# Kernel optimization log

Hardware: AMD Instinct MI355X
Metric: run time of the kernel (lower is better)

The kernel has to match this reference:

```python
import jax, jax.numpy as jnp
import numpy as np

N_NODES = 100000
N_EDGES = 1600000
NUM_FEATURES = 64
HIDDEN = 64
NUM_CLASSES = 16


def setup_inputs() -> dict:
    key = jax.random.key(0)
    ks = jax.random.split(key, 8)
    x = jax.random.normal(ks[0], (N_NODES, NUM_FEATURES), dtype=jnp.float32)
    edge_index = jax.random.randint(ks[1], (2, N_EDGES), 0, N_NODES, dtype=jnp.int32)
    # Glorot-ish init for weights, zero bias (matches GCNConv / Linear defaults closely enough)
    s1 = 1.0 / np.sqrt(NUM_FEATURES)
    s2 = 1.0 / np.sqrt(HIDDEN)
    W1 = jax.random.uniform(ks[2], (NUM_FEATURES, HIDDEN), jnp.float32, -s1, s1)
    b1 = jnp.zeros((HIDDEN,), jnp.float32)
    W2 = jax.random.uniform(ks[3], (HIDDEN, HIDDEN), jnp.float32, -s2, s2)
    b2 = jnp.zeros((HIDDEN,), jnp.float32)
    W3 = jax.random.uniform(ks[4], (HIDDEN, NUM_CLASSES), jnp.float32, -s2, s2)
    b3 = jax.random.uniform(ks[5], (NUM_CLASSES,), jnp.float32, -s2, s2)
    return {"x": x, "edge_index": edge_index, "W1": W1, "b1": b1,
            "W2": W2, "b2": b2, "W3": W3, "b3": b3}


def _gcn_layer(x, W, b, src, dst, norm, n_nodes):
    # GCNConv: h = X W; out[i] = sum_{(j->i)} norm_ji * h[j]; out += b
    h = x @ W                                   # [N, H] small dense GEMM
    msg = h[src] * norm[:, None]                # [E+N, H] irregular gather
    out = jax.ops.segment_sum(msg, dst, num_segments=n_nodes)  # scatter-add
    return out + b


def reference(x, edge_index, W1, b1, W2, b2, W3, b3):
    n = x.shape[0]
    loop = jnp.arange(n, dtype=edge_index.dtype)
    # add self-loops (PyG GCNConv default add_self_loops=True)
    src = jnp.concatenate([edge_index[0], loop])
    dst = jnp.concatenate([edge_index[1], loop])
    # symmetric normalization D^{-1/2} A_hat D^{-1/2}
    deg = jax.ops.segment_sum(jnp.ones_like(src, dtype=x.dtype), dst, num_segments=n)
    dis = jax.lax.rsqrt(deg)                    # deg >= 1 due to self-loops
    norm = dis[src] * dis[dst]                  # [E+N]

    h = jax.nn.relu(_gcn_layer(x, W1, b1, src, dst, norm, n))
    # F.dropout(training=False) -> identity (module in eval mode)
    h = jax.nn.relu(_gcn_layer(h, W2, b2, src, dst, norm, n))
    z = h @ W3 + b3
    return jax.nn.log_softmax(z, axis=1), h
```

## Files before the change

### kernel.cpp

```cpp
#include <hip/hip_runtime.h>
#include <hip/hip_bf16.h>

typedef __hip_bfloat16 bf16;
typedef unsigned short ushort;

#define NN 100000
#define NE 1600000
#define NBKT 391
#define BCAP 4608
#define EPB 4096
#define NP1 391
#define NMT 6250

typedef __attribute__((ext_vector_type(8))) short s8v;
typedef __attribute__((ext_vector_type(4))) float f4v;

__device__ __forceinline__ float ldf(const void* p, int i, int f32) {
    return f32 ? ((const float*)p)[i] : __bfloat162float(((const bf16*)p)[i]);
}
__device__ __forceinline__ void stf(void* p, int i, int f32, float v) {
    if (f32) ((float*)p)[i] = v;
    else     ((bf16*)p)[i] = __float2bfloat16(v);
}

__device__ __forceinline__ ushort f2b(float f) {
    unsigned u = __builtin_bit_cast(unsigned, f);
    u += 0x7FFF + ((u >> 16) & 1);
    return (ushort)(u >> 16);
}
__device__ __forceinline__ float b2f(ushort h) {
    unsigned u = ((unsigned)h) << 16;
    return __builtin_bit_cast(float, u);
}
__device__ __forceinline__ float blo(unsigned u) {
    return __builtin_bit_cast(float, u << 16);
}
__device__ __forceinline__ float bhi(unsigned u) {
    return __builtin_bit_cast(float, u & 0xffff0000u);
}

__global__ void k_detect(const unsigned* __restrict__ x, int* __restrict__ flag) {
    __shared__ int cnt[256];
    int t = threadIdx.x, c = 0;
    for (int i = t; i < 2048; i += 256) {
        unsigned e7 = (x[i] >> 8) & 0x7F;
        c += (e7 >= 60 && e7 <= 66) ? 1 : 0;
    }
    cnt[t] = c;
    __syncthreads();
    for (int s = 128; s > 0; s >>= 1) {
        if (t < s) cnt[t] += cnt[t + s];
        __syncthreads();
    }
    if (t == 0) *flag = (cnt[0] >= 1024) ? 0 : 1;
}

__global__ void k_sentinel(unsigned* out) {
    if (threadIdx.x == 0 && blockIdx.x == 0) out[0] = 0x461C461Cu;
}

__global__ void k_cnt(const int* __restrict__ dst, int* __restrict__ cnt) {
    __shared__ int hist[NBKT];
    int b = blockIdx.x, t = threadIdx.x;
    for (int i = t; i < NBKT; i += 256) hist[i] = 0;
    __syncthreads();
    int e0 = b * EPB;
#pragma unroll
    for (int k = 0; k < EPB; k += 256) {
        int e = e0 + k + t;
        if (e < NE) atomicAdd(&hist[dst[e] >> 8], 1);
    }
    __syncthreads();
    for (int i = t; i < NBKT; i += 256) cnt[b * NBKT + i] = hist[i];
}

__global__ void k_colscan(const int* __restrict__ cnt, int* __restrict__ prefT,
                          int* __restrict__ btot) {
    __shared__ int s[512];
    int k = blockIdx.x, t = threadIdx.x;
    int v = (t < NP1) ? cnt[t * NBKT + k] : 0;
    s[t] = v;
    __syncthreads();
    for (int d = 1; d < 512; d <<= 1) {
        int add = (t >= d) ? s[t - d] : 0;
        __syncthreads();
        s[t] += add;
        __syncthreads();
    }
    if (t < NP1) prefT[k * NP1 + t] = s[t] - v;
    if (t == 511) btot[k] = s[511];
}

__global__ void k_scanB(const int* __restrict__ btot, int* __restrict__ gbase,
                        int* __restrict__ rowptr) {
    __shared__ int s[512];
    int t = threadIdx.x;
    int v = (t < NBKT) ? btot[t] : 0;
    s[t] = v;
    __syncthreads();
    for (int d = 1; d < 512; d <<= 1) {
        int add = (t >= d) ? s[t - d] : 0;
        __syncthreads();
        s[t] += add;
        __syncthreads();
    }
    if (t < NBKT) gbase[t] = s[t] - v;
    if (t == 0) { gbase[NBKT] = NE; rowptr[NN] = NE; }
}

__global__ void k_place(const int* __restrict__ src, const int* __restrict__ dst,
                        const int* __restrict__ prefT, unsigned* __restrict__ bbuf) {
    __shared__ int base[NBKT];
    __shared__ int lcur[NBKT];
    int b = blockIdx.x, t = threadIdx.x;
    for (int i = t; i < NBKT; i += 256) {
        base[i] = prefT[i * NP1 + b];
        lcur[i] = 0;
    }
    __syncthreads();
    int e0 = b * EPB;
#pragma unroll
    for (int k = 0; k < EPB; k += 256) {
        int e = e0 + k + t;
        if (e < NE) {
            int d = dst[e];
            int kb = d >> 8;
            int lp = atomicAdd(&lcur[kb], 1);
            bbuf[kb * BCAP + base[kb] + lp] = ((unsigned)src[e] << 8) | (unsigned)(d & 255);
        }
    }
}

__global__ void k_pass2(const unsigned* __restrict__ bbuf, const int* __restrict__ gbase,
                        int* __restrict__ rowptr, float* __restrict__ dis,
                        int* __restrict__ csr_off) {
    __shared__ unsigned vals[BCAP];
    __shared__ int lout[BCAP];
    __shared__ int fh[256], fx[256], fc[256];
    int b = blockIdx.x, t = threadIdx.x;
    int g0 = gbase[b], cntb = gbase[b + 1] - g0;
    const unsigned* in = bbuf + b * BCAP;
    fh[t] = 0;
    __syncthreads();
    for (int i = t; i < cntb; i += 256) {
        unsigned v = in[i];
        vals[i] = v;
        atomicAdd(&fh[v & 255], 1);
    }
    __syncthreads();
    fx[t] = fh[t];
    __syncthreads();
    for (int d = 1; d < 256; d <<= 1) {
        int add = (t >= d) ? fx[t - d] : 0;
        __syncthreads();
        fx[t] += add;
        __syncthreads();
    }
    int n = b * 256 + t;
    int ex = fx[t] - fh[t];
    fc[t] = ex;
    if (n < NN) {
        rowptr[n] = g0 + ex;
        dis[n] = rsqrtf(1.0f + (float)fh[t]);
    }
    __syncthreads();
    for (int i = t; i < cntb; i += 256) {
        unsigned v = vals[i];
        int p = atomicAdd(&fc[v & 255], 1);
        lout[p] = (int)((v >> 8) << 7);
    }
    __syncthreads();
    for (int i = t; i < cntb; i += 256) csr_off[g0 + i] = lout[i];
}

__global__ void __launch_bounds__(256) k_gemm_mfma(
        const void* __restrict__ A, int aBase, const void* __restrict__ W,
        bf16* __restrict__ C, const float* __restrict__ dis,
        const int* __restrict__ flag) {
    int f32 = *flag;
    int t = threadIdx.x;
    if (blockIdx.x == 0 && t < 64) ((ushort*)C)[NN * 64 + t] = 0;
    int lane = t & 63;
    int w = t >> 6;
    int m = lane & 15, q = lane >> 4;

    s8v bh[2][4], bl[2][4];
#pragma unroll
    for (int st = 0; st < 2; st++)
#pragma unroll
        for (int nt = 0; nt < 4; nt++)
#pragma unroll
            for (int j = 0; j < 8; j++) {
                int k = st * 32 + q * 8 + j;
                float wv = ldf(W, k * 64 + nt * 16 + m, f32);
                ushort h = f2b(wv);
                bh[st][nt][j] = (short)h;
                bl[st][nt][j] = (short)f2b(wv - b2f(h));
            }

    ushort* Cu = (ushort*)C;
    int gw = blockIdx.x * 4 + w;
    int nw = gridDim.x * 4;
    for (int mt = gw; mt < NMT; mt += nw) {
        int row = mt * 16 + m;
        s8v ah[2], al[2];
        if (f32) {
            const float* ap = (const float*)A + aBase + row * 64 + q * 8;
#pragma unroll
            for (int st = 0; st < 2; st++)
#pragma unroll
                for (int j = 0; j < 8; j++) {
                    float v = ap[st * 32 + j];
                    ushort h = f2b(v);
                    ah[st][j] = (short)h;
                    al[st][j] = (short)f2b(v - b2f(h));
                }
        } else {
            const short* ap = (const short*)A + aBase + row * 64 + q * 8;
            ah[0] = *(const s8v*)(ap);
            ah[1] = *(const s8v*)(ap + 32);
        }
        float dr[4];
#pragma unroll
        for (int r = 0; r < 4; r++) dr[r] = dis[mt * 16 + q * 4 + r];
#pragma unroll
        for (int nt = 0; nt < 4; nt++) {
            f4v acc = {0.f, 0.f, 0.f, 0.f};
#pragma unroll
            for (int st = 0; st < 2; st++)
                acc = __builtin_amdgcn_mfma_f32_16x16x32_bf16(ah[st], bh[st][nt], acc, 0, 0, 0);
            if (f32) {
#pragma unroll
                for (int st = 0; st < 2; st++) {
                    acc = __builtin_amdgcn_mfma_f32_16x16x32_bf16(ah[st], bl[st][nt], acc, 0, 0, 0);
                    acc = __builtin_amdgcn_mfma_f32_16x16x32_bf16(al[st], bh[st][nt], acc, 0, 0, 0);
                }
            }
            int col = nt * 16 + m;
#pragma unroll
            for (int r = 0; r < 4; r++) {
                int rr = mt * 16 + q * 4 + r;
                Cu[rr * 64 + col] = f2b(dr[r] * acc[r]);
            }
        }
    }
}

__global__ void __launch_bounds__(256, 4) k_aggregate(
        const bf16* __restrict__ hs, void* hout, int hoBase,
        const float* __restrict__ dis,
        const int* __restrict__ rowptr,
        const int* __restrict__ csr_off,
        const void* __restrict__ bias,
        const int* __restrict__ flag) {
    int f32 = *flag;
    int t = threadIdx.x;
    int n = blockIdx.x * 4 + (t >> 6);
    if (n >= NN) return;
    int l = t & 63;
    int q = l >> 4;
    int m = l & 15;
    int fb = m * 8;
    const char* hb = (const char*)hs;
    int r0 = rowptr[n], r1 = rowptr[n + 1];
    float a0 = 0.f, a1 = 0.f, a2 = 0.f, a3 = 0.f;
    int j = r0;
    for (; j + 16 <= r1; j += 16) {
        int o0 = csr_off[j + q];
        int o1 = csr_off[j + 4 + q];
        int o2 = csr_off[j + 8 + q];
        int o3 = csr_off[j + 12 + q];
        uint2 v0 = *(const uint2*)(hb + o0 + fb);
        uint2 v1 = *(const uint2*)(hb + o1 + fb);
        uint2 v2 = *(const uint2*)(hb + o2 + fb);
        uint2 v3 = *(const uint2*)(hb + o3 + fb);
        a0 += blo(v0.x); a1 += bhi(v0.x); a2 += blo(v0.y); a3 += bhi(v0.y);
        a0 += blo(v1.x); a1 += bhi(v1.x); a2 += blo(v1.y); a3 += bhi(v1.y);
        a0 += blo(v2.x); a1 += bhi(v2.x); a2 += blo(v2.y); a3 += bhi(v2.y);
        a0 += blo(v3.x); a1 += bhi(v3.x); a2 += blo(v3.y); a3 += bhi(v3.y);
    }
    if (j < r1) {
        const int Z = NN * 128;
        int i0 = j + q, i1 = j + 4 + q, i2 = j + 8 + q, i3 = j + 12 + q;
        int o0 = csr_off[i0]; o0 = (i0 < r1) ? o0 : Z;
        int o1 = csr_off[i1]; o1 = (i1 < r1) ? o1 : Z;
        int o2 = csr_off[i2]; o2 = (i2 < r1) ? o2 : Z;
        int o3 = csr_off[i3]; o3 = (i3 < r1) ? o3 : Z;
        uint2 v0 = *(const uint2*)(hb + o0 + fb);
        uint2 v1 = *(const uint2*)(hb + o1 + fb);
        uint2 v2 = *(const uint2*)(hb + o2 + fb);
        uint2 v3 = *(const uint2*)(hb + o3 + fb);
        a0 += blo(v0.x); a1 += bhi(v0.x); a2 += blo(v0.y); a3 += bhi(v0.y);
        a0 += blo(v1.x); a1 += bhi(v1.x); a2 += blo(v1.y); a3 += bhi(v1.y);
        a0 += blo(v2.x); a1 += bhi(v2.x); a2 += blo(v2.y); a3 += bhi(v2.y);
        a0 += blo(v3.x); a1 += bhi(v3.x); a2 += blo(v3.y); a3 += bhi(v3.y);
    }
    a0 += __shfl_xor(a0, 32); a1 += __shfl_xor(a1, 32);
    a2 += __shfl_xor(a2, 32); a3 += __shfl_xor(a3, 32);
    a0 += __shfl_xor(a0, 16); a1 += __shfl_xor(a1, 16);
    a2 += __shfl_xor(a2, 16); a3 += __shfl_xor(a3, 16);
    if (q == 0) {
        uint2 sv = *(const uint2*)(hb + n * 128 + fb);
        float dn = dis[n];
        float b0 = ldf(bias, m * 4 + 0, f32);
        float b1v = ldf(bias, m * 4 + 1, f32);
        float b2v = ldf(bias, m * 4 + 2, f32);
        float b3v = ldf(bias, m * 4 + 3, f32);
        float o0 = fmaxf(dn * (a0 + blo(sv.x)) + b0, 0.f);
        float o1 = fmaxf(dn * (a1 + bhi(sv.x)) + b1v, 0.f);
        float o2 = fmaxf(dn * (a2 + blo(sv.y)) + b2v, 0.f);
        float o3 = fmaxf(dn * (a3 + bhi(sv.y)) + b3v, 0.f);
        if (f32) {
            float4 ov = {o0, o1, o2, o3};
            *(float4*)((float*)hout + hoBase + n * 64 + m * 4) = ov;
        } else {
            unsigned w0 = (unsigned)f2b(o0) | ((unsigned)f2b(o1) << 16);
            unsigned w1 = (unsigned)f2b(o2) | ((unsigned)f2b(o3) << 16);
            uint2 wv; wv.x = w0; wv.y = w1;
            *(uint2*)((ushort*)hout + hoBase + n * 64 + m * 4) = wv;
        }
    }
}

__global__ void k_head(const void* __restrict__ h2, int hBase,
                       const void* __restrict__ W3, const void* __restrict__ b3,
                       void* out, const int* __restrict__ flag) {
    __shared__ float w[64 * 16];
    __shared__ float hrow[16 * 64];
    int f32 = *flag;
    int t = threadIdx.x;
#pragma unroll
    for (int i = 0; i < 4; i++) w[t + i * 256] = ldf(W3, t + i * 256, f32);
    int r0 = blockIdx.x * 16;
#pragma unroll
    for (int i = 0; i < 4; i++) hrow[t + i * 256] = ldf(h2, hBase + r0 * 64 + t + i * 256, f32);
    __syncthreads();
    int lr = t >> 4, c = t & 15;
    float z = ldf(b3, c, f32);
#pragma unroll
    for (int k = 0; k < 64; k++) z += hrow[lr * 64 + k] * w[k * 16 + c];
    float m = z;
#pragma unroll
    for (int off = 8; off >= 1; off >>= 1) m = fmaxf(m, __shfl_xor(m, off, 16));
    float p = expf(z - m);
    float s = p;
#pragma unroll
    for (int off = 8; off >= 1; off >>= 1) s += __shfl_xor(s, off, 16);
    stf(out, (r0 + lr) * 16 + c, f32, z - m - logf(s));
}

extern "C" void kernel_launch(void* const* d_in, const int* in_sizes, int n_in,
                              void* d_out, int out_size, void* d_ws, size_t ws_size,
                              hipStream_t stream) {
    const void* x  = d_in[0];
    const int* ei  = (const int*)d_in[1];
    const void* W1 = d_in[2];
    const void* b1 = d_in[3];
    const void* W2 = d_in[4];
    const void* b2 = d_in[5];
    const void* W3 = d_in[6];
    const void* b3 = d_in[7];

    const size_t NEEDED = (size_t)(1807104 + 3203072) * 4;
    if (ws_size < NEEDED) {
        k_sentinel<<<1, 64, 0, stream>>>((unsigned*)d_out);
        return;
    }
    int*      flag    = (int*)d_ws;
    float*    dis     = (float*)d_ws + 256;
    int*      rowptr  = (int*)d_ws + 102656;
    int*      gbase   = (int*)d_ws + 205056;
    int*      btot    = (int*)d_ws + 205568;
    int*      csr_off = (int*)d_ws + 207104;
    unsigned* bbuf    = (unsigned*)((int*)d_ws + 1807104);
    int*      cnt     = (int*)d_ws + 1807104 + NBKT * BCAP;
    int*      prefT   = cnt + 153088;
    bf16*     bufA    = (bf16*)bbuf;

    const int* srcp = ei;
    const int* dstp = ei + NE;
    const int HB = NN * 16;

    k_detect<<<1, 256, 0, stream>>>((const unsigned*)x, flag);

    k_cnt<<<NP1, 256, 0, stream>>>(dstp, cnt);
    k_colscan<<<NBKT, 512, 0, stream>>>(cnt, prefT, btot);
    k_scanB<<<1, 512, 0, stream>>>(btot, gbase, rowptr);
    k_place<<<NP1, 256, 0, stream>>>(srcp, dstp, prefT, bbuf);
    k_pass2<<<NBKT, 256, 0, stream>>>(bbuf, gbase, rowptr, dis, csr_off);

    k_gemm_mfma<<<512, 256, 0, stream>>>(x, 0, W1, bufA, dis, flag);
    k_aggregate<<<NN / 4, 256, 0, stream>>>(bufA, d_out, HB, dis, rowptr, csr_off, b1, flag);

    k_gemm_mfma<<<512, 256, 0, stream>>>(d_out, HB, W2, bufA, dis, flag);
    k_aggregate<<<NN / 4, 256, 0, stream>>>(bufA, d_out, HB, dis, rowptr, csr_off, b2, flag);

    k_head<<<NN / 16, 256, 0, stream>>>(d_out, HB, W3, b3, d_out, flag);
}
```

Before: 269.4 us.

## Fold detect and bucket-scan kernels into neighbors; persistent grid-stride aggregation

Removes the separate dtype-detect kernel by running it in block 0 of the count kernel. Removes the single-block bucket scan by having each pass2 block reduce the preceding bucket totals itself. The aggregation kernel becomes a grid-stride persistent loop over 2048 blocks with 8-wave launch bounds, bias loads hoisted out of the loop, and packed float2 accumulation. Together these cut launch count and per-block setup, in exchange for redundant prefix reductions in pass2 and possible load imbalance in the persistent loop.

```diff
diff --git a/kernel.cpp b/kernel.cpp
--- a/kernel.cpp
+++ b/kernel.cpp
@@ -14,6 +14,7 @@
 
 typedef __attribute__((ext_vector_type(8))) short s8v;
 typedef __attribute__((ext_vector_type(4))) float f4v;
+typedef __attribute__((ext_vector_type(2))) float f2v;
 
 __device__ __forceinline__ float ldf(const void* p, int i, int f32) {
     return f32 ? ((const float*)p)[i] : __bfloat162float(((const bf16*)p)[i]);
@@ -38,28 +39,16 @@
 __device__ __forceinline__ float bhi(unsigned u) {
     return __builtin_bit_cast(float, u & 0xffff0000u);
 }
-
-__global__ void k_detect(const unsigned* __restrict__ x, int* __restrict__ flag) {
-    __shared__ int cnt[256];
-    int t = threadIdx.x, c = 0;
-    for (int i = t; i < 2048; i += 256) {
-        unsigned e7 = (x[i] >> 8) & 0x7F;
-        c += (e7 >= 60 && e7 <= 66) ? 1 : 0;
-    }
-    cnt[t] = c;
-    __syncthreads();
-    for (int s = 128; s > 0; s >>= 1) {
-        if (t < s) cnt[t] += cnt[t + s];
-        __syncthreads();
-    }
-    if (t == 0) *flag = (cnt[0] >= 1024) ? 0 : 1;
+__device__ __forceinline__ f2v up2(unsigned u) {
+    f2v r; r.x = blo(u); r.y = bhi(u); return r;
 }
 
 __global__ void k_sentinel(unsigned* out) {
     if (threadIdx.x == 0 && blockIdx.x == 0) out[0] = 0x461C461Cu;
 }
 
-__global__ void k_cnt(const int* __restrict__ dst, int* __restrict__ cnt) {
+__global__ void k_cnt(const unsigned* __restrict__ x, int* __restrict__ flag,
+                      const int* __restrict__ dst, int* __restrict__ cnt) {
     __shared__ int hist[NBKT];
     int b = blockIdx.x, t = threadIdx.x;
     for (int i = t; i < NBKT; i += 256) hist[i] = 0;
@@ -72,6 +61,21 @@
     }
     __syncthreads();
     for (int i = t; i < NBKT; i += 256) cnt[b * NBKT + i] = hist[i];
+    if (b == 0) {
+        int c = 0;
+        for (int i = t; i < 2048; i += 256) {
+            unsigned e7 = (x[i] >> 8) & 0x7F;
+            c += (e7 >= 60 && e7 <= 66) ? 1 : 0;
+        }
+        __syncthreads();
+        hist[t] = c;
+        __syncthreads();
+        for (int s = 128; s > 0; s >>= 1) {
+            if (t < s) hist[t] += hist[t + s];
+            __syncthreads();
+        }
+        if (t == 0) *flag = (hist[0] >= 1024) ? 0 : 1;
+    }
 }
 
 __global__ void k_colscan(const int* __restrict__ cnt, int* __restrict__ prefT,
@@ -89,23 +93,6 @@
     }
     if (t < NP1) prefT[k * NP1 + t] = s[t] - v;
     if (t == 511) btot[k] = s[511];
-}
-
-__global__ void k_scanB(const int* __restrict__ btot, int* __restrict__ gbase,
-                        int* __restrict__ rowptr) {
-    __shared__ int s[512];
-    int t = threadIdx.x;
-    int v = (t < NBKT) ? btot[t] : 0;
-    s[t] = v;
-    __syncthreads();
-    for (int d = 1; d < 512; d <<= 1) {
-        int add = (t >= d) ? s[t - d] : 0;
-        __syncthreads();
-        s[t] += add;
-        __syncthreads();
-    }
-    if (t < NBKT) gbase[t] = s[t] - v;
-    if (t == 0) { gbase[NBKT] = NE; rowptr[NN] = NE; }
 }
 
 __global__ void k_place(const int* __restrict__ src, const int* __restrict__ dst,
@@ -131,14 +118,25 @@
     }
 }
 
-__global__ void k_pass2(const unsigned* __restrict__ bbuf, const int* __restrict__ gbase,
+__global__ void k_pass2(const unsigned* __restrict__ bbuf, const int* __restrict__ btot,
                         int* __restrict__ rowptr, float* __restrict__ dis,
                         int* __restrict__ csr_off) {
     __shared__ unsigned vals[BCAP];
     __shared__ int lout[BCAP];
     __shared__ int fh[256], fx[256], fc[256];
     int b = blockIdx.x, t = threadIdx.x;
-    int g0 = gbase[b], cntb = gbase[b + 1] - g0;
+    int part = 0;
+    for (int i = t; i < b; i += 256) part += btot[i];
+    fh[t] = part;
+    __syncthreads();
+    for (int s = 128; s > 0; s >>= 1) {
+        if (t < s) fh[t] += fh[t + s];
+        __syncthreads();
+    }
+    int g0 = fh[0];
+    int cntb = btot[b];
+    if (b == 0 && t == 0) rowptr[NN] = NE;
+    __syncthreads();
     const unsigned* in = bbuf + b * BCAP;
     fh[t] = 0;
     __syncthreads();
@@ -246,7 +244,7 @@
     }
 }
 
-__global__ void __launch_bounds__(256, 4) k_aggregate(
+__global__ void __launch_bounds__(256, 8) k_aggregate(
         const bf16* __restrict__ hs, void* hout, int hoBase,
         const float* __restrict__ dis,
         const int* __restrict__ rowptr,
@@ -255,69 +253,72 @@
         const int* __restrict__ flag) {
     int f32 = *flag;
     int t = threadIdx.x;
-    int n = blockIdx.x * 4 + (t >> 6);
-    if (n >= NN) return;
     int l = t & 63;
     int q = l >> 4;
     int m = l & 15;
     int fb = m * 8;
     const char* hb = (const char*)hs;
-    int r0 = rowptr[n], r1 = rowptr[n + 1];
-    float a0 = 0.f, a1 = 0.f, a2 = 0.f, a3 = 0.f;
-    int j = r0;
-    for (; j + 16 <= r1; j += 16) {
-        int o0 = csr_off[j + q];
-        int o1 = csr_off[j + 4 + q];
-        int o2 = csr_off[j + 8 + q];
-        int o3 = csr_off[j + 12 + q];
-        uint2 v0 = *(const uint2*)(hb + o0 + fb);
-        uint2 v1 = *(const uint2*)(hb + o1 + fb);
-        uint2 v2 = *(const uint2*)(hb + o2 + fb);
-        uint2 v3 = *(const uint2*)(hb + o3 + fb);
-        a0 += blo(v0.x); a1 += bhi(v0.x); a2 += blo(v0.y); a3 += bhi(v0.y);
-        a0 += blo(v1.x); a1 += bhi(v1.x); a2 += blo(v1.y); a3 += bhi(v1.y);
-        a0 += blo(v2.x); a1 += bhi(v2.x); a2 += blo(v2.y); a3 += bhi(v2.y);
-        a0 += blo(v3.x); a1 += bhi(v3.x); a2 += blo(v3.y); a3 += bhi(v3.y);
-    }
-    if (j < r1) {
-        const int Z = NN * 128;
-        int i0 = j + q, i1 = j + 4 + q, i2 = j + 8 + q, i3 = j + 12 + q;
-        int o0 = csr_off[i0]; o0 = (i0 < r1) ? o0 : Z;
-        int o1 = csr_off[i1]; o1 = (i1 < r1) ? o1 : Z;
-        int o2 = csr_off[i2]; o2 = (i2 < r1) ? o2 : Z;
-        int o3 = csr_off[i3]; o3 = (i3 < r1) ? o3 : Z;
-        uint2 v0 = *(const uint2*)(hb + o0 + fb);
-        uint2 v1 = *(const uint2*)(hb + o1 + fb);
-        uint2 v2 = *(const uint2*)(hb + o2 + fb);
-        uint2 v3 = *(const uint2*)(hb + o3 + fb);
-        a0 += blo(v0.x); a1 += bhi(v0.x); a2 += blo(v0.y); a3 += bhi(v0.y);
-        a0 += blo(v1.x); a1 += bhi(v1.x); a2 += blo(v1.y); a3 += bhi(v1.y);
-        a0 += blo(v2.x); a1 += bhi(v2.x); a2 += blo(v2.y); a3 += bhi(v2.y);
-        a0 += blo(v3.x); a1 += bhi(v3.x); a2 += blo(v3.y); a3 += bhi(v3.y);
-    }
-    a0 += __shfl_xor(a0, 32); a1 += __shfl_xor(a1, 32);
-    a2 += __shfl_xor(a2, 32); a3 += __shfl_xor(a3, 32);
-    a0 += __shfl_xor(a0, 16); a1 += __shfl_xor(a1, 16);
-    a2 += __shfl_xor(a2, 16); a3 += __shfl_xor(a3, 16);
-    if (q == 0) {
-        uint2 sv = *(const uint2*)(hb + n * 128 + fb);
-        float dn = dis[n];
-        float b0 = ldf(bias, m * 4 + 0, f32);
-        float b1v = ldf(bias, m * 4 + 1, f32);
-        float b2v = ldf(bias, m * 4 + 2, f32);
-        float b3v = ldf(bias, m * 4 + 3, f32);
-        float o0 = fmaxf(dn * (a0 + blo(sv.x)) + b0, 0.f);
-        float o1 = fmaxf(dn * (a1 + bhi(sv.x)) + b1v, 0.f);
-        float o2 = fmaxf(dn * (a2 + blo(sv.y)) + b2v, 0.f);
-        float o3 = fmaxf(dn * (a3 + bhi(sv.y)) + b3v, 0.f);
-        if (f32) {
-            float4 ov = {o0, o1, o2, o3};
-            *(float4*)((float*)hout + hoBase + n * 64 + m * 4) = ov;
-        } else {
-            unsigned w0 = (unsigned)f2b(o0) | ((unsigned)f2b(o1) << 16);
-            unsigned w1 = (unsigned)f2b(o2) | ((unsigned)f2b(o3) << 16);
-            uint2 wv; wv.x = w0; wv.y = w1;
-            *(uint2*)((ushort*)hout + hoBase + n * 64 + m * 4) = wv;
+    float b0 = ldf(bias, m * 4 + 0, f32);
+    float b1v = ldf(bias, m * 4 + 1, f32);
+    float b2v = ldf(bias, m * 4 + 2, f32);
+    float b3v = ldf(bias, m * 4 + 3, f32);
+    const int Z = NN * 128;
+    int wid = blockIdx.x * 4 + (t >> 6);
+    int nwav = gridDim.x * 4;
+    for (int n = wid; n < NN; n += nwav) {
+        int r0 = rowptr[n], r1 = rowptr[n + 1];
+        f2v a01 = {0.f, 0.f}, a23 = {0.f, 0.f};
+        int j = r0;
+        for (; j + 16 <= r1; j += 16) {
+            int o0 = csr_off[j + q];
+            int o1 = csr_off[j + 4 + q];
+            int o2 = csr_off[j + 8 + q];
+            int o3 = csr_off[j + 12 + q];
+            uint2 v0 = *(const uint2*)(hb + o0 + fb);
+            uint2 v1 = *(const uint2*)(hb + o1 + fb);
+            uint2 v2 = *(const uint2*)(hb + o2 + fb);
+            uint2 v3 = *(const uint2*)(hb + o3 + fb);
+            a01 += up2(v0.x); a23 += up2(v0.y);
+            a01 += up2(v1.x); a23 += up2(v1.y);
+            a01 += up2(v2.x); a23 += up2(v2.y);
+            a01 += up2(v3.x); a23 += up2(v3.y);
+        }
+        if (j < r1) {
+            int i0 = j + q, i1 = j + 4 + q, i2 = j + 8 + q, i3 = j + 12 + q;
+            int o0 = csr_off[i0]; o0 = (i0 < r1) ? o0 : Z;
+            int o1 = csr_off[i1]; o1 = (i1 < r1) ? o1 : Z;
+            int o2 = csr_off[i2]; o2 = (i2 < r1) ? o2 : Z;
+            int o3 = csr_off[i3]; o3 = (i3 < r1) ? o3 : Z;
+            uint2 v0 = *(const uint2*)(hb + o0 + fb);
+            uint2 v1 = *(const uint2*)(hb + o1 + fb);
+            uint2 v2 = *(const uint2*)(hb + o2 + fb);
+            uint2 v3 = *(const uint2*)(hb + o3 + fb);
+            a01 += up2(v0.x); a23 += up2(v0.y);
+            a01 += up2(v1.x); a23 += up2(v1.y);
+            a01 += up2(v2.x); a23 += up2(v2.y);
+            a01 += up2(v3.x); a23 += up2(v3.y);
+        }
+        float a0 = a01.x, a1 = a01.y, a2 = a23.x, a3 = a23.y;
+        a0 += __shfl_xor(a0, 32); a1 += __shfl_xor(a1, 32);
+        a2 += __shfl_xor(a2, 32); a3 += __shfl_xor(a3, 32);
+        a0 += __shfl_xor(a0, 16); a1 += __shfl_xor(a1, 16);
+        a2 += __shfl_xor(a2, 16); a3 += __shfl_xor(a3, 16);
+        if (q == 0) {
+            uint2 sv = *(const uint2*)(hb + n * 128 + fb);
+            float dn = dis[n];
+            float o0 = fmaxf(dn * (a0 + blo(sv.x)) + b0, 0.f);
+            float o1 = fmaxf(dn * (a1 + bhi(sv.x)) + b1v, 0.f);
+            float o2 = fmaxf(dn * (a2 + blo(sv.y)) + b2v, 0.f);
+            float o3 = fmaxf(dn * (a3 + bhi(sv.y)) + b3v, 0.f);
+            if (f32) {
+                float4 ov = {o0, o1, o2, o3};
+                *(float4*)((float*)hout + hoBase + n * 64 + m * 4) = ov;
+            } else {
+                unsigned w0 = (unsigned)f2b(o0) | ((unsigned)f2b(o1) << 16);
+                unsigned w1 = (unsigned)f2b(o2) | ((unsigned)f2b(o3) << 16);
+                uint2 wv; wv.x = w0; wv.y = w1;
+                *(uint2*)((ushort*)hout + hoBase + n * 64 + m * 4) = wv;
+            }
         }
     }
 }
@@ -369,7 +370,6 @@
     int*      flag    = (int*)d_ws;
     float*    dis     = (float*)d_ws + 256;
     int*      rowptr  = (int*)d_ws + 102656;
-    int*      gbase   = (int*)d_ws + 205056;
     int*      btot    = (int*)d_ws + 205568;
     int*      csr_off = (int*)d_ws + 207104;
     unsigned* bbuf    = (unsigned*)((int*)d_ws + 1807104);
@@ -381,19 +381,16 @@
     const int* dstp = ei + NE;
     const int HB = NN * 16;
 
-    k_detect<<<1, 256, 0, stream>>>((const unsigned*)x, flag);
-
-    k_cnt<<<NP1, 256, 0, stream>>>(dstp, cnt);
+    k_cnt<<<NP1, 256, 0, stream>>>((const unsigned*)x, flag, dstp, cnt);
     k_colscan<<<NBKT, 512, 0, stream>>>(cnt, prefT, btot);
-    k_scanB<<<1, 512, 0, stream>>>(btot, gbase, rowptr);
     k_place<<<NP1, 256, 0, stream>>>(srcp, dstp, prefT, bbuf);
-    k_pass2<<<NBKT, 256, 0, stream>>>(bbuf, gbase, rowptr, dis, csr_off);
+    k_pass2<<<NBKT, 256, 0, stream>>>(bbuf, btot, rowptr, dis, csr_off);
 
     k_gemm_mfma<<<512, 256, 0, stream>>>(x, 0, W1, bufA, dis, flag);
-    k_aggregate<<<NN / 4, 256, 0, stream>>>(bufA, d_out, HB, dis, rowptr, csr_off, b1, flag);
+    k_aggregate<<<2048, 256, 0, stream>>>(bufA, d_out, HB, dis, rowptr, csr_off, b1, flag);
 
     k_gemm_mfma<<<512, 256, 0, stream>>>(d_out, HB, W2, bufA, dis, flag);
-    k_aggregate<<<NN / 4, 256, 0, stream>>>(bufA, d_out, HB, dis, rowptr, csr_off, b2, flag);
+    k_aggregate<<<2048, 256, 0, stream>>>(bufA, d_out, HB, dis, rowptr, csr_off, b2, flag);
 
     k_head<<<NN / 16, 256, 0, stream>>>(d_out, HB, W3, b3, d_out, flag);
 }
```

New measurement: 254.5 us. -5.5%, faster.
